# Optimization experiments

Measured on AMD Instinct MI355X. Metric: run time of the kernel, lower is better.

The kernel has to match this reference:

```python
import jax, jax.numpy as jnp
import numpy as np

H = 1024        # hidden_size
V = 50257       # output_size (vocab)
L = 2048        # number of encoder annotations


def setup_inputs() -> dict:
    key = jax.random.key(0)
    ks = jax.random.split(key, 24)
    s = 0.02
    inp = {
        "input_tok": jax.random.randint(ks[0], (1,), 0, V),
        "hidden": jax.random.normal(ks[1], (1, H), jnp.float32),
        "encoder_outputs": jax.random.normal(ks[2], (L, 1, 2 * H), jnp.float32),
        "cell_state": jax.random.normal(ks[3], (1, H), jnp.float32),
        # embedding: Linear(V, H)
        "W_emb": jax.random.normal(ks[4], (V, H), jnp.float32) * s,
        "b_emb": jnp.zeros((H,), jnp.float32),
        # attn_layer: Linear(3H, H); attn_output: Linear(H, 1)
        "W_attn": jax.random.normal(ks[5], (3 * H, H), jnp.float32) * s,
        "b_attn": jnp.zeros((H,), jnp.float32),
        "W_attn_out": jax.random.normal(ks[6], (H, 1), jnp.float32) * s,
        "b_attn_out": jnp.zeros((1,), jnp.float32),
        # LSTM gates: Linear(3H + H, H) each
        "W_i": jax.random.normal(ks[7], (4 * H, H), jnp.float32) * s,
        "b_i": jnp.zeros((H,), jnp.float32),
        "W_o": jax.random.normal(ks[8], (4 * H, H), jnp.float32) * s,
        "b_o": jnp.zeros((H,), jnp.float32),
        "W_f": jax.random.normal(ks[9], (4 * H, H), jnp.float32) * s,
        "b_f": jnp.zeros((H,), jnp.float32),
        "W_c": jax.random.normal(ks[10], (4 * H, H), jnp.float32) * s,
        "b_c": jnp.zeros((H,), jnp.float32),
        # output_layer: Linear(4H, V)
        "W_out": jax.random.normal(ks[11], (4 * H, V), jnp.float32) * s,
        "b_out": jnp.zeros((V,), jnp.float32),
    }
    return inp


def reference(input_tok, hidden, encoder_outputs, cell_state,
              W_emb, b_emb, W_attn, b_attn, W_attn_out, b_attn_out,
              W_i, b_i, W_o, b_o, W_f, b_f, W_c, b_c, W_out, b_out):
    # embedding of one-hot previous token: [1, V] @ [V, H] -> [1, H]
    one_hot = jax.nn.one_hot(input_tok, V, dtype=W_emb.dtype)
    emb = one_hot @ W_emb + b_emb                     # [1, H]
    # dropout_p = 0.0 -> identity (eval-mode reference)

    enc = encoder_outputs[:, 0, :]                    # [L, 2H]
    hid_b = jnp.broadcast_to(hidden, (enc.shape[0], hidden.shape[1]))
    attn_in = jnp.concatenate([enc, hid_b], axis=1)   # [L, 3H]
    scores = jnp.tanh(attn_in @ W_attn + b_attn) @ W_attn_out + b_attn_out  # [L, 1]
    # exp(e_ij) / sum_j exp(e_ij)  ==  softmax over encoder steps
    attn_weights = jax.nn.softmax(scores, axis=0)     # [L, 1]
    context = jnp.sum(attn_weights * enc, axis=0, keepdims=True)  # [1, 2H]

    # LSTM step on cat(embedding, context) with state (hidden, cell_state)
    lstm_in = jnp.concatenate([emb, context], axis=1)              # [1, 3H]
    combined = jnp.concatenate([lstm_in, hidden], axis=1)          # [1, 4H]
    i_g = jax.nn.sigmoid(combined @ W_i + b_i)
    o_g = jax.nn.sigmoid(combined @ W_o + b_o)
    f_g = jax.nn.sigmoid(combined @ W_f + b_f)
    c_g = jnp.tanh(combined @ W_c + b_c)
    new_cell = f_g * cell_state + i_g * c_g
    next_hidden = o_g * jnp.tanh(new_cell)

    out = jnp.concatenate([emb, hidden, context], axis=1) @ W_out + b_out  # [1, V]
    log_softmax = jax.nn.log_softmax(out, axis=1)
    return (log_softmax, next_hidden, attn_weights, new_cell)
```

## Files before the change

kernel.cpp:

```cpp
#include <hip/hip_runtime.h>
#include <hip/hip_bf16.h>
#include <math.h>

#define Hh 1024
#define Vv 50257
#define Ll 2048
#define H2 2048
#define H4 4096

#define WS_EMB  0
#define WS_SC   1024
#define WS_CTX  3072
#define WS_GATE 5120
#define WS_LOG  9216
#define WS_PAIR 59474
#define WS_LOGZ 59868
#define WS_HB   59872
#define OA_BYTES 245760u
#define OB_BYTES 8634368u

#define OUT_NH Vv
#define OUT_AW (Vv + 1024)
#define OUT_NC (Vv + 3072)

typedef __attribute__((ext_vector_type(8))) short bf16x8;
typedef __attribute__((ext_vector_type(4))) float f32x4;
typedef __attribute__((ext_vector_type(4), aligned(4))) float f32x4u;

__device__ __forceinline__ float sigmoidf_(float x) { return 1.f / (1.f + expf(-x)); }
__device__ __forceinline__ unsigned short f2bf(float f) {
    union { float f; unsigned u; } v; v.f = f;
    unsigned r = v.u + 0x7FFF + ((v.u >> 16) & 1);
    return (unsigned short)(r >> 16);
}

__global__ void k1_prep(const int* __restrict__ tok, const float* __restrict__ W_emb,
                        const float* __restrict__ b_emb, const float* __restrict__ b_out,
                        const float* __restrict__ b_attn, float* __restrict__ ws) {
    int i = blockIdx.x * 256 + threadIdx.x;
    if (i < Hh)  ws[WS_EMB + i] = W_emb[(size_t)tok[0] * Hh + i] + b_emb[i];
    if (i < Hh)  ws[WS_HB + i] = b_attn[i];
    if (i < Ll)  ws[WS_SC + i] = 0.f;
    if (i < H2)  ws[WS_CTX + i] = 0.f;
    if (i < H4)  ws[WS_GATE + i] = 0.f;
    if (i < Vv)  ws[WS_LOG + i] = b_out[i];
}

__global__ __launch_bounds__(256) void kPrep(const float* __restrict__ enc,
        const float* __restrict__ W_attn, const float* __restrict__ hidden,
        float* __restrict__ ws, char* __restrict__ wsb) {
    __shared__ union { float a[16][132]; float b[32][68]; } sh;
    int bx = blockIdx.x;
    int t = threadIdx.x;
    if (bx < 2048) {
        int mt = bx >> 4, kc = bx & 15;
        {
            int row = t >> 4, c8 = (t & 15) * 8;
            const float* src = enc + (size_t)(mt * 16 + row) * H2 + kc * 128 + c8;
            float4 v0 = *(const float4*)src;
            float4 v1 = *(const float4*)(src + 4);
            *(float4*)&sh.a[row][c8] = v0;
            *(float4*)&sh.a[row][c8 + 4] = v1;
        }
        __syncthreads();
        int ktl = t >> 6, l = t & 63;
        int r2 = l & 15, k8 = (l >> 4) * 8;
        bf16x8 o;
#pragma unroll
        for (int j = 0; j < 8; ++j) o[j] = (short)f2bf(sh.a[r2][ktl * 32 + k8 + j]);
        *(bf16x8*)(wsb + OA_BYTES + ((size_t)(mt * 64 + kc * 4 + ktl)) * 1024 + l * 16) = o;
    } else if (bx < 3072) {
        int bxx = bx - 2048;
        int kt = bxx >> 4, nc = bxx & 15;
        {
            int r = t >> 3, c8 = (t & 7) * 8;
            const float* src = W_attn + (size_t)(kt * 32 + r) * Hh + nc * 64 + c8;
            float4 v0 = *(const float4*)src;
            float4 v1 = *(const float4*)(src + 4);
            *(float4*)&sh.b[r][c8] = v0;
            *(float4*)&sh.b[r][c8 + 4] = v1;
        }
        __syncthreads();
        int ntl = t >> 6, l = t & 63;
        int col = ntl * 16 + (l & 15), k8 = (l >> 4) * 8;
        bf16x8 o;
#pragma unroll
        for (int j = 0; j < 8; ++j) o[j] = (short)f2bf(sh.b[k8 + j][col]);
        *(bf16x8*)(wsb + OB_BYTES + ((size_t)((nc * 4 + ntl) * 64 + kt)) * 1024 + l * 16) = o;
    } else {
        int bxx = bx - 3072;
        int hc = bxx & 3, kc = bxx >> 2;
        int h = hc * 256 + t;
        int k0 = kc * 16;
        const float* p = W_attn + (size_t)(H2 + k0) * Hh + h;
        float acc = 0.f;
#pragma unroll
        for (int k = 0; k < 16; ++k) { acc += hidden[k0 + k] * __builtin_nontemporal_load(p); p += Hh; }
        atomicAdd(&ws[WS_HB + h], acc);
    }
}

__global__ __launch_bounds__(128, 1) void kG(const char* __restrict__ wsb,
        const float* __restrict__ Wo, float* __restrict__ ws) {
    int bx = blockIdx.x;
    int bm = bx >> 4, bn = bx & 15;
    int t = threadIdx.x, w = t >> 6, l = t & 63;
    int mt0 = bm * 4 + w * 2;
    int nt0 = bn * 4;
    const char* pa0 = wsb + OA_BYTES + (size_t)(mt0)     * 65536 + l * 16;
    const char* pa1 = wsb + OA_BYTES + (size_t)(mt0 + 1) * 65536 + l * 16;
    const char* pb0 = wsb + OB_BYTES + (size_t)(nt0)     * 65536 + l * 16;
    const char* pb1 = wsb + OB_BYTES + (size_t)(nt0 + 1) * 65536 + l * 16;
    const char* pb2 = wsb + OB_BYTES + (size_t)(nt0 + 2) * 65536 + l * 16;
    const char* pb3 = wsb + OB_BYTES + (size_t)(nt0 + 3) * 65536 + l * 16;

    f32x4 acc[2][4];
#pragma unroll
    for (int i = 0; i < 2; ++i)
#pragma unroll
        for (int j = 0; j < 4; ++j) acc[i][j] = (f32x4){0.f, 0.f, 0.f, 0.f};

    bf16x8 As[8][2], Bs[8][4];
#define LOADK(s, kk) { int o_ = (kk) * 1024; \
    As[s][0] = *(const bf16x8*)(pa0 + o_); As[s][1] = *(const bf16x8*)(pa1 + o_); \
    Bs[s][0] = *(const bf16x8*)(pb0 + o_); Bs[s][1] = *(const bf16x8*)(pb1 + o_); \
    Bs[s][2] = *(const bf16x8*)(pb2 + o_); Bs[s][3] = *(const bf16x8*)(pb3 + o_); }
#define MFMAK(s) { \
    _Pragma("unroll") for (int mr = 0; mr < 2; ++mr) \
    _Pragma("unroll") for (int nr = 0; nr < 4; ++nr) \
        acc[mr][nr] = __builtin_amdgcn_mfma_f32_16x16x32_bf16(As[s][mr], Bs[s][nr], acc[mr][nr], 0, 0, 0); }

    LOADK(0, 0) LOADK(1, 1) LOADK(2, 2) LOADK(3, 3)
    LOADK(4, 4) LOADK(5, 5) LOADK(6, 6) LOADK(7, 7)
    for (int kt = 0; kt < 56; kt += 8) {
        MFMAK(0) LOADK(0, kt + 8)
        MFMAK(1) LOADK(1, kt + 9)
        MFMAK(2) LOADK(2, kt + 10)
        MFMAK(3) LOADK(3, kt + 11)
        MFMAK(4) LOADK(4, kt + 12)
        MFMAK(5) LOADK(5, kt + 13)
        MFMAK(6) LOADK(6, kt + 14)
        MFMAK(7) LOADK(7, kt + 15)
    }
    MFMAK(0) MFMAK(1) MFMAK(2) MFMAK(3) MFMAK(4) MFMAK(5) MFMAK(6) MFMAK(7)
#undef LOADK
#undef MFMAK

    float sp[8];
#pragma unroll
    for (int i = 0; i < 8; ++i) sp[i] = 0.f;
    int nlane = bn * 64 + (l & 15);
#pragma unroll
    for (int nr = 0; nr < 4; ++nr) {
        int n = nlane + nr * 16;
        float hb = ws[WS_HB + n];
        float wo = Wo[n];
#pragma unroll
        for (int mr = 0; mr < 2; ++mr)
#pragma unroll
            for (int r = 0; r < 4; ++r)
                sp[mr * 4 + r] += tanhf(acc[mr][nr][r] + hb) * wo;
    }
#pragma unroll
    for (int m = 1; m <= 8; m <<= 1)
#pragma unroll
        for (int i = 0; i < 8; ++i) sp[i] += __shfl_xor(sp[i], m, 64);
    if ((l & 15) == 0) {
        int mbase = bm * 64 + w * 32 + (l >> 4) * 4;
#pragma unroll
        for (int mr = 0; mr < 2; ++mr)
#pragma unroll
            for (int r = 0; r < 4; ++r)
                atomicAdd(&ws[WS_SC + mbase + mr * 16 + r], sp[mr * 4 + r]);
    }
}

__global__ __launch_bounds__(256) void k34(const float* __restrict__ enc,
        float* __restrict__ ws, float* __restrict__ out) {
    __shared__ float red[256];
    __shared__ float wl[64];
    int b = blockIdx.x, t = threadIdx.x;
    int jc = b & 7, lc = b >> 3;
    float s[8];
    float mx = -INFINITY;
#pragma unroll
    for (int i = 0; i < 8; ++i) { s[i] = ws[WS_SC + i * 256 + t]; mx = fmaxf(mx, s[i]); }
    red[t] = mx;
    __syncthreads();
    for (int off = 128; off > 0; off >>= 1) {
        if (t < off) red[t] = fmaxf(red[t], red[t + off]);
        __syncthreads();
    }
    float M = red[0];
    __syncthreads();
    float se = 0.f;
#pragma unroll
    for (int i = 0; i < 8; ++i) se += expf(s[i] - M);
    red[t] = se;
    __syncthreads();
    for (int off = 128; off > 0; off >>= 1) {
        if (t < off) red[t] += red[t + off];
        __syncthreads();
    }
    float invZ = 1.f / red[0];
    int l0 = lc * 64;
    if (t < 64) wl[t] = expf(ws[WS_SC + l0 + t] - M) * invZ;
    __syncthreads();
    if (jc == 0 && t < 64) out[OUT_AW + l0 + t] = wl[t];
    int j = jc * 256 + t;
    float acc = 0.f;
#pragma unroll 8
    for (int i = 0; i < 64; ++i)
        acc += wl[i] * enc[(size_t)(l0 + i) * H2 + j];
    atomicAdd(&ws[WS_CTX + j], acc);
}

__global__ __launch_bounds__(256) void k5k7(const float* __restrict__ W_out,
        const float* __restrict__ W_i, const float* __restrict__ W_o,
        const float* __restrict__ W_f, const float* __restrict__ W_c,
        const float* __restrict__ hidden, float* __restrict__ ws) {
    int bx = blockIdx.x, t = threadIdx.x;
    if (bx < 800) {
        __shared__ float xs[256];
        int vb = bx % 50, kc = bx / 50;
        int k0 = kc * 256;
        {
            int k = k0 + t;
            xs[t] = (k < 1024) ? ws[WS_EMB + k] : (k < 2048) ? hidden[k - 1024] : ws[WS_CTX + (k - 2048)];
        }
        __syncthreads();
        int v4 = vb * 1024 + t * 4;
        if (v4 + 3 < Vv) {
            const char* p = (const char*)(W_out + (size_t)k0 * Vv + v4);
            f32x4 a = (f32x4){0.f, 0.f, 0.f, 0.f};
#pragma unroll 4
            for (int i = 0; i < 256; ++i) {
                f32x4u wv = __builtin_nontemporal_load((const f32x4u*)p);
                a += wv * xs[i];
                p += (size_t)Vv * 4;
            }
            atomicAdd(&ws[WS_LOG + v4 + 0], a.x);
            atomicAdd(&ws[WS_LOG + v4 + 1], a.y);
            atomicAdd(&ws[WS_LOG + v4 + 2], a.z);
            atomicAdd(&ws[WS_LOG + v4 + 3], a.w);
        } else if (v4 < Vv) {
            for (int jj = 0; jj < 4 && v4 + jj < Vv; ++jj) {
                const float* p = W_out + (size_t)k0 * Vv + v4 + jj;
                float a = 0.f;
                for (int i = 0; i < 256; ++i) { a += xs[i] * (*p); p += Vv; }
                atomicAdd(&ws[WS_LOG + v4 + jj], a);
            }
        }
    } else {
        int bxx = bx - 800;
        int g = bxx & 3, kc = bxx >> 2;
        int k0 = kc * 32;
        const float* Wm = (g == 0) ? W_i : (g == 1) ? W_o : (g == 2) ? W_f : W_c;
        const f32x4* p = (const f32x4*)(Wm + (size_t)k0 * Hh) + t;
        f32x4 a = (f32x4){0.f, 0.f, 0.f, 0.f};
#pragma unroll 8
        for (int k = k0; k < k0 + 32; ++k) {
            float x = (k < 1024) ? ws[WS_EMB + k] : (k < 3072) ? ws[WS_CTX + (k - 1024)] : hidden[k - 3072];
            f32x4 wv = __builtin_nontemporal_load(p);
            a += wv * x;
            p += 256;
        }
        int h4 = t * 4;
        atomicAdd(&ws[WS_GATE + g * 1024 + h4 + 0], a.x);
        atomicAdd(&ws[WS_GATE + g * 1024 + h4 + 1], a.y);
        atomicAdd(&ws[WS_GATE + g * 1024 + h4 + 2], a.z);
        atomicAdd(&ws[WS_GATE + g * 1024 + h4 + 3], a.w);
    }
}

__global__ __launch_bounds__(256) void k6k8a(const float* __restrict__ b_i,
        const float* __restrict__ b_o, const float* __restrict__ b_f,
        const float* __restrict__ b_c, const float* __restrict__ cell,
        float* __restrict__ ws, float* __restrict__ out) {
    int bx = blockIdx.x, t = threadIdx.x;
    if (bx < 197) {
        __shared__ float sm[256];
        int v = bx * 256 + t;
        float x = (v < Vv) ? ws[WS_LOG + v] : -INFINITY;
        sm[t] = x;
        __syncthreads();
        for (int off = 128; off > 0; off >>= 1) {
            if (t < off) sm[t] = fmaxf(sm[t], sm[t + off]);
            __syncthreads();
        }
        float m = sm[0];
        __syncthreads();
        sm[t] = (v < Vv) ? expf(x - m) : 0.f;
        __syncthreads();
        for (int off = 128; off > 0; off >>= 1) {
            if (t < off) sm[t] += sm[t + off];
            __syncthreads();
        }
        if (t == 0) { ws[WS_PAIR + 2 * bx] = m; ws[WS_PAIR + 2 * bx + 1] = sm[0]; }
    } else {
#pragma unroll
        for (int r = 0; r < 4; ++r) {
            int h = t + r * 256;
            float ig = sigmoidf_(ws[WS_GATE + h] + b_i[h]);
            float og = sigmoidf_(ws[WS_GATE + 1024 + h] + b_o[h]);
            float fg = sigmoidf_(ws[WS_GATE + 2048 + h] + b_f[h]);
            float cg = tanhf(ws[WS_GATE + 3072 + h] + b_c[h]);
            float nc = fg * cell[h] + ig * cg;
            out[OUT_NC + h] = nc;
            out[OUT_NH + h] = og * tanhf(nc);
        }
    }
}

__global__ __launch_bounds__(256) void k8bc(const float* __restrict__ ws, float* __restrict__ out) {
    __shared__ float sm[256], ss[256];
    int t = threadIdx.x;
    float m = (t < 197) ? ws[WS_PAIR + 2 * t] : -INFINITY;
    float s = (t < 197) ? ws[WS_PAIR + 2 * t + 1] : 0.f;
    sm[t] = m;
    __syncthreads();
    for (int off = 128; off > 0; off >>= 1) {
        if (t < off) sm[t] = fmaxf(sm[t], sm[t + off]);
        __syncthreads();
    }
    float M = sm[0];
    ss[t] = s * expf(m - M);
    __syncthreads();
    for (int off = 128; off > 0; off >>= 1) {
        if (t < off) ss[t] += ss[t + off];
        __syncthreads();
    }
    float logZ = M + logf(ss[0]);
    int v = blockIdx.x * 256 + t;
    if (v < Vv) out[v] = ws[WS_LOG + v] - logZ;
}

extern "C" void kernel_launch(void* const* d_in, const int* in_sizes, int n_in,
                              void* d_out, int out_size, void* d_ws, size_t ws_size,
                              hipStream_t stream) {
    const int*   tok        = (const int*)d_in[0];
    const float* hidden     = (const float*)d_in[1];
    const float* enc        = (const float*)d_in[2];
    const float* cell       = (const float*)d_in[3];
    const float* W_emb      = (const float*)d_in[4];
    const float* b_emb      = (const float*)d_in[5];
    const float* W_attn     = (const float*)d_in[6];
    const float* b_attn     = (const float*)d_in[7];
    const float* W_attn_out = (const float*)d_in[8];
    const float* W_i   = (const float*)d_in[10];
    const float* b_i   = (const float*)d_in[11];
    const float* W_o   = (const float*)d_in[12];
    const float* b_o   = (const float*)d_in[13];
    const float* W_f   = (const float*)d_in[14];
    const float* b_f   = (const float*)d_in[15];
    const float* W_c   = (const float*)d_in[16];
    const float* b_c   = (const float*)d_in[17];
    const float* W_out = (const float*)d_in[18];
    const float* b_out = (const float*)d_in[19];
    float* out = (float*)d_out;
    float* ws  = (float*)d_ws;
    char*  wsb = (char*)d_ws;

    k1_prep<<<dim3(197), dim3(256), 0, stream>>>(tok, W_emb, b_emb, b_out, b_attn, ws);
    kPrep<<<dim3(3328), dim3(256), 0, stream>>>(enc, W_attn, hidden, ws, wsb);
    kG<<<dim3(512), dim3(128), 0, stream>>>(wsb, W_attn_out, ws);
    k34<<<dim3(256), dim3(256), 0, stream>>>(enc, ws, out);
    k5k7<<<dim3(1312), dim3(256), 0, stream>>>(W_out, W_i, W_o, W_f, W_c, hidden, ws);
    k6k8a<<<dim3(198), dim3(256), 0, stream>>>(b_i, b_o, b_f, b_c, cell, ws, out);
    k8bc<<<dim3(197), dim3(256), 0, stream>>>(ws, out);
}
```

Baseline: 224.7 us.

## Spread W_out streaming across earlier kernels and replace logit atomics with partials

The large W_out GEMV, previously one phase after the attention pipeline, is split by K-chunk. Each chunk is issued inside whichever earlier kernel already has its input available: hidden and embedding chunks go in the prep kernels, embedding chunks also share the MFMA scoring kernel and the softmax/context kernel, and context chunks go in the gate kernel. This overlaps the bandwidth-bound weight stream with the attention GEMM and softmax stages. The atomic accumulation into the logits is replaced by per-chunk partial rows in workspace, which the log-softmax kernel sums together with b_out. The cost is extra workspace traffic for 16 partial rows and heterogeneous blocks that may unbalance the compute-bound kernels.

Result: slower. 291.5 us (+29.7%).

```diff
diff --git a/kernel.cpp b/kernel.cpp
--- a/kernel.cpp
+++ b/kernel.cpp
@@ -14,10 +14,11 @@
 #define WS_GATE 5120
 #define WS_LOG  9216
 #define WS_PAIR 59474
-#define WS_LOGZ 59868
 #define WS_HB   59872
 #define OA_BYTES 245760u
 #define OB_BYTES 8634368u
+#define PP 50264
+#define WS_PART_F 3210240
 
 #define OUT_NH Vv
 #define OUT_AW (Vv + 1024)
@@ -34,24 +35,56 @@
     return (unsigned short)(r >> 16);
 }
 
-__global__ void k1_prep(const int* __restrict__ tok, const float* __restrict__ W_emb,
-                        const float* __restrict__ b_emb, const float* __restrict__ b_out,
-                        const float* __restrict__ b_attn, float* __restrict__ ws) {
-    int i = blockIdx.x * 256 + threadIdx.x;
-    if (i < Hh)  ws[WS_EMB + i] = W_emb[(size_t)tok[0] * Hh + i] + b_emb[i];
-    if (i < Hh)  ws[WS_HB + i] = b_attn[i];
-    if (i < Ll)  ws[WS_SC + i] = 0.f;
-    if (i < H2)  ws[WS_CTX + i] = 0.f;
-    if (i < H4)  ws[WS_GATE + i] = 0.f;
-    if (i < Vv)  ws[WS_LOG + i] = b_out[i];
-}
-
-__global__ __launch_bounds__(256) void kPrep(const float* __restrict__ enc,
+__device__ __forceinline__ void stream_wout(const float* __restrict__ W_out,
+        const float* __restrict__ xs, int k0, int v4, float* __restrict__ part_row) {
+    if (v4 + 3 < Vv) {
+        const char* p = (const char*)(W_out + (size_t)k0 * Vv + v4);
+        f32x4 a = (f32x4){0.f, 0.f, 0.f, 0.f};
+#pragma unroll 4
+        for (int i = 0; i < 256; ++i) {
+            f32x4u wv = __builtin_nontemporal_load((const f32x4u*)p);
+            a += wv * xs[i];
+            p += (size_t)Vv * 4;
+        }
+        __builtin_nontemporal_store(a, (f32x4u*)(part_row + v4));
+    } else if (v4 < Vv) {
+        for (int jj = 0; jj < 4 && v4 + jj < Vv; ++jj) {
+            const float* p = W_out + (size_t)k0 * Vv + v4 + jj;
+            float a = 0.f;
+            for (int i = 0; i < 256; ++i) { a += xs[i] * (*p); p += Vv; }
+            part_row[v4 + jj] = a;
+        }
+    }
+}
+
+__global__ __launch_bounds__(256) void kA(const int* __restrict__ tok,
+        const float* __restrict__ W_emb, const float* __restrict__ b_emb,
+        const float* __restrict__ b_attn, const float* __restrict__ hidden,
+        const float* __restrict__ W_out, float* __restrict__ ws) {
+    __shared__ float xs[256];
+    int bx = blockIdx.x, t = threadIdx.x;
+    if (bx < 16) {
+        int i = bx * 256 + t;
+        if (i < Hh) { ws[WS_EMB + i] = W_emb[(size_t)tok[0] * Hh + i] + b_emb[i];
+                      ws[WS_HB + i] = b_attn[i]; }
+        if (i < Ll)  ws[WS_SC + i] = 0.f;
+        if (i < H2)  ws[WS_CTX + i] = 0.f;
+        if (i < H4)  ws[WS_GATE + i] = 0.f;
+    } else {
+        int s = bx - 16;
+        int kc = 4 + s / 50, vb = s % 50;
+        int k0 = kc * 256;
+        xs[t] = hidden[k0 - 1024 + t];
+        __syncthreads();
+        stream_wout(W_out, xs, k0, vb * 1024 + t * 4, ws + WS_PART_F + (size_t)kc * PP);
+    }
+}
+
+__global__ __launch_bounds__(256) void kB(const float* __restrict__ enc,
         const float* __restrict__ W_attn, const float* __restrict__ hidden,
-        float* __restrict__ ws, char* __restrict__ wsb) {
-    __shared__ union { float a[16][132]; float b[32][68]; } sh;
-    int bx = blockIdx.x;
-    int t = threadIdx.x;
+        const float* __restrict__ W_out, float* __restrict__ ws, char* __restrict__ wsb) {
+    __shared__ union { float a[16][132]; float b[32][68]; float xs[256]; } sh;
+    int bx = blockIdx.x, t = threadIdx.x;
     if (bx < 2048) {
         int mt = bx >> 4, kc = bx & 15;
         {
@@ -87,7 +120,7 @@
 #pragma unroll
         for (int j = 0; j < 8; ++j) o[j] = (short)f2bf(sh.b[k8 + j][col]);
         *(bf16x8*)(wsb + OB_BYTES + ((size_t)((nc * 4 + ntl) * 64 + kt)) * 1024 + l * 16) = o;
-    } else {
+    } else if (bx < 3328) {
         int bxx = bx - 3072;
         int hc = bxx & 3, kc = bxx >> 2;
         int h = hc * 256 + t;
@@ -97,30 +130,41 @@
 #pragma unroll
         for (int k = 0; k < 16; ++k) { acc += hidden[k0 + k] * __builtin_nontemporal_load(p); p += Hh; }
         atomicAdd(&ws[WS_HB + h], acc);
-    }
-}
-
-__global__ __launch_bounds__(128, 1) void kG(const char* __restrict__ wsb,
-        const float* __restrict__ Wo, float* __restrict__ ws) {
-    int bx = blockIdx.x;
-    int bm = bx >> 4, bn = bx & 15;
-    int t = threadIdx.x, w = t >> 6, l = t & 63;
-    int mt0 = bm * 4 + w * 2;
-    int nt0 = bn * 4;
-    const char* pa0 = wsb + OA_BYTES + (size_t)(mt0)     * 65536 + l * 16;
-    const char* pa1 = wsb + OA_BYTES + (size_t)(mt0 + 1) * 65536 + l * 16;
-    const char* pb0 = wsb + OB_BYTES + (size_t)(nt0)     * 65536 + l * 16;
-    const char* pb1 = wsb + OB_BYTES + (size_t)(nt0 + 1) * 65536 + l * 16;
-    const char* pb2 = wsb + OB_BYTES + (size_t)(nt0 + 2) * 65536 + l * 16;
-    const char* pb3 = wsb + OB_BYTES + (size_t)(nt0 + 3) * 65536 + l * 16;
-
-    f32x4 acc[2][4];
-#pragma unroll
-    for (int i = 0; i < 2; ++i)
-#pragma unroll
-        for (int j = 0; j < 4; ++j) acc[i][j] = (f32x4){0.f, 0.f, 0.f, 0.f};
-
-    bf16x8 As[8][2], Bs[8][4];
+    } else {
+        int s = bx - 3328;
+        int kc = (s < 50) ? 7 : 0;
+        int vb = s % 50;
+        int k0 = kc * 256;
+        sh.xs[t] = (kc == 7) ? hidden[768 + t] : ws[WS_EMB + t];
+        __syncthreads();
+        stream_wout(W_out, sh.xs, k0, vb * 1024 + t * 4, ws + WS_PART_F + (size_t)kc * PP);
+    }
+}
+
+__global__ __launch_bounds__(128, 1) void kC(const char* __restrict__ wsb,
+        const float* __restrict__ Wo, const float* __restrict__ W_out,
+        float* __restrict__ ws) {
+    __shared__ float xs[256];
+    int bx = blockIdx.x, t = threadIdx.x;
+    if (bx < 512) {
+        int bm = bx >> 4, bn = bx & 15;
+        int w = t >> 6, l = t & 63;
+        int mt0 = bm * 4 + w * 2;
+        int nt0 = bn * 4;
+        const char* pa0 = wsb + OA_BYTES + (size_t)(mt0)     * 65536 + l * 16;
+        const char* pa1 = wsb + OA_BYTES + (size_t)(mt0 + 1) * 65536 + l * 16;
+        const char* pb0 = wsb + OB_BYTES + (size_t)(nt0)     * 65536 + l * 16;
+        const char* pb1 = wsb + OB_BYTES + (size_t)(nt0 + 1) * 65536 + l * 16;
+        const char* pb2 = wsb + OB_BYTES + (size_t)(nt0 + 2) * 65536 + l * 16;
+        const char* pb3 = wsb + OB_BYTES + (size_t)(nt0 + 3) * 65536 + l * 16;
+
+        f32x4 acc[2][4];
+#pragma unroll
+        for (int i = 0; i < 2; ++i)
+#pragma unroll
+            for (int j = 0; j < 4; ++j) acc[i][j] = (f32x4){0.f, 0.f, 0.f, 0.f};
+
+        bf16x8 As[8][2], Bs[8][4];
 #define LOADK(s, kk) { int o_ = (kk) * 1024; \
     As[s][0] = *(const bf16x8*)(pa0 + o_); As[s][1] = *(const bf16x8*)(pa1 + o_); \
     Bs[s][0] = *(const bf16x8*)(pb0 + o_); Bs[s][1] = *(const bf16x8*)(pb1 + o_); \
@@ -130,129 +174,122 @@
     _Pragma("unroll") for (int nr = 0; nr < 4; ++nr) \
         acc[mr][nr] = __builtin_amdgcn_mfma_f32_16x16x32_bf16(As[s][mr], Bs[s][nr], acc[mr][nr], 0, 0, 0); }
 
-    LOADK(0, 0) LOADK(1, 1) LOADK(2, 2) LOADK(3, 3)
-    LOADK(4, 4) LOADK(5, 5) LOADK(6, 6) LOADK(7, 7)
-    for (int kt = 0; kt < 56; kt += 8) {
-        MFMAK(0) LOADK(0, kt + 8)
-        MFMAK(1) LOADK(1, kt + 9)
-        MFMAK(2) LOADK(2, kt + 10)
-        MFMAK(3) LOADK(3, kt + 11)
-        MFMAK(4) LOADK(4, kt + 12)
-        MFMAK(5) LOADK(5, kt + 13)
-        MFMAK(6) LOADK(6, kt + 14)
-        MFMAK(7) LOADK(7, kt + 15)
-    }
-    MFMAK(0) MFMAK(1) MFMAK(2) MFMAK(3) MFMAK(4) MFMAK(5) MFMAK(6) MFMAK(7)
+        LOADK(0, 0) LOADK(1, 1) LOADK(2, 2) LOADK(3, 3)
+        LOADK(4, 4) LOADK(5, 5) LOADK(6, 6) LOADK(7, 7)
+        for (int kt = 0; kt < 56; kt += 8) {
+            MFMAK(0) LOADK(0, kt + 8)
+            MFMAK(1) LOADK(1, kt + 9)
+            MFMAK(2) LOADK(2, kt + 10)
+            MFMAK(3) LOADK(3, kt + 11)
+            MFMAK(4) LOADK(4, kt + 12)
+            MFMAK(5) LOADK(5, kt + 13)
+            MFMAK(6) LOADK(6, kt + 14)
+            MFMAK(7) LOADK(7, kt + 15)
+        }
+        MFMAK(0) MFMAK(1) MFMAK(2) MFMAK(3) MFMAK(4) MFMAK(5) MFMAK(6) MFMAK(7)
 #undef LOADK
 #undef MFMAK
 
-    float sp[8];
-#pragma unroll
-    for (int i = 0; i < 8; ++i) sp[i] = 0.f;
-    int nlane = bn * 64 + (l & 15);
-#pragma unroll
-    for (int nr = 0; nr < 4; ++nr) {
-        int n = nlane + nr * 16;
-        float hb = ws[WS_HB + n];
-        float wo = Wo[n];
-#pragma unroll
-        for (int mr = 0; mr < 2; ++mr)
-#pragma unroll
-            for (int r = 0; r < 4; ++r)
-                sp[mr * 4 + r] += tanhf(acc[mr][nr][r] + hb) * wo;
-    }
-#pragma unroll
-    for (int m = 1; m <= 8; m <<= 1)
-#pragma unroll
-        for (int i = 0; i < 8; ++i) sp[i] += __shfl_xor(sp[i], m, 64);
-    if ((l & 15) == 0) {
-        int mbase = bm * 64 + w * 32 + (l >> 4) * 4;
-#pragma unroll
-        for (int mr = 0; mr < 2; ++mr)
-#pragma unroll
-            for (int r = 0; r < 4; ++r)
-                atomicAdd(&ws[WS_SC + mbase + mr * 16 + r], sp[mr * 4 + r]);
-    }
-}
-
-__global__ __launch_bounds__(256) void k34(const float* __restrict__ enc,
-        float* __restrict__ ws, float* __restrict__ out) {
+        float sp[8];
+#pragma unroll
+        for (int i = 0; i < 8; ++i) sp[i] = 0.f;
+        int nlane = bn * 64 + (l & 15);
+#pragma unroll
+        for (int nr = 0; nr < 4; ++nr) {
+            int n = nlane + nr * 16;
+            float hb = ws[WS_HB + n];
+            float wo = Wo[n];
+#pragma unroll
+            for (int mr = 0; mr < 2; ++mr)
+#pragma unroll
+                for (int r = 0; r < 4; ++r)
+                    sp[mr * 4 + r] += tanhf(acc[mr][nr][r] + hb) * wo;
+        }
+#pragma unroll
+        for (int m = 1; m <= 8; m <<= 1)
+#pragma unroll
+            for (int i = 0; i < 8; ++i) sp[i] += __shfl_xor(sp[i], m, 64);
+        if ((l & 15) == 0) {
+            int mbase = bm * 64 + w * 32 + (l >> 4) * 4;
+#pragma unroll
+            for (int mr = 0; mr < 2; ++mr)
+#pragma unroll
+                for (int r = 0; r < 4; ++r)
+                    atomicAdd(&ws[WS_SC + mbase + mr * 16 + r], sp[mr * 4 + r]);
+        }
+    } else {
+        int s = bx - 512;
+        int kc = 1 + s / 99, vb = s % 99;
+        int k0 = kc * 256;
+        xs[t] = ws[WS_EMB + k0 + t];
+        xs[t + 128] = ws[WS_EMB + k0 + t + 128];
+        __syncthreads();
+        stream_wout(W_out, xs, k0, vb * 512 + t * 4, ws + WS_PART_F + (size_t)kc * PP);
+    }
+}
+
+__global__ __launch_bounds__(256) void kD(const float* __restrict__ enc,
+        const float* __restrict__ W_out, float* __restrict__ ws, float* __restrict__ out) {
     __shared__ float red[256];
     __shared__ float wl[64];
-    int b = blockIdx.x, t = threadIdx.x;
-    int jc = b & 7, lc = b >> 3;
-    float s[8];
-    float mx = -INFINITY;
-#pragma unroll
-    for (int i = 0; i < 8; ++i) { s[i] = ws[WS_SC + i * 256 + t]; mx = fmaxf(mx, s[i]); }
-    red[t] = mx;
-    __syncthreads();
-    for (int off = 128; off > 0; off >>= 1) {
-        if (t < off) red[t] = fmaxf(red[t], red[t + off]);
-        __syncthreads();
-    }
-    float M = red[0];
-    __syncthreads();
-    float se = 0.f;
-#pragma unroll
-    for (int i = 0; i < 8; ++i) se += expf(s[i] - M);
-    red[t] = se;
-    __syncthreads();
-    for (int off = 128; off > 0; off >>= 1) {
-        if (t < off) red[t] += red[t + off];
-        __syncthreads();
-    }
-    float invZ = 1.f / red[0];
-    int l0 = lc * 64;
-    if (t < 64) wl[t] = expf(ws[WS_SC + l0 + t] - M) * invZ;
-    __syncthreads();
-    if (jc == 0 && t < 64) out[OUT_AW + l0 + t] = wl[t];
-    int j = jc * 256 + t;
-    float acc = 0.f;
+    __shared__ float xs[256];
+    int bx = blockIdx.x, t = threadIdx.x;
+    if (bx < 256) {
+        int jc = bx & 7, lc = bx >> 3;
+        float s[8];
+        float mx = -INFINITY;
+#pragma unroll
+        for (int i = 0; i < 8; ++i) { s[i] = ws[WS_SC + i * 256 + t]; mx = fmaxf(mx, s[i]); }
+        red[t] = mx;
+        __syncthreads();
+        for (int off = 128; off > 0; off >>= 1) {
+            if (t < off) red[t] = fmaxf(red[t], red[t + off]);
+            __syncthreads();
+        }
+        float M = red[0];
+        __syncthreads();
+        float se = 0.f;
+#pragma unroll
+        for (int i = 0; i < 8; ++i) se += expf(s[i] - M);
+        red[t] = se;
+        __syncthreads();
+        for (int off = 128; off > 0; off >>= 1) {
+            if (t < off) red[t] += red[t + off];
+            __syncthreads();
+        }
+        float invZ = 1.f / red[0];
+        int l0 = lc * 64;
+        if (t < 64) wl[t] = expf(ws[WS_SC + l0 + t] - M) * invZ;
+        __syncthreads();
+        if (jc == 0 && t < 64) out[OUT_AW + l0 + t] = wl[t];
+        int j = jc * 256 + t;
+        float acc = 0.f;
 #pragma unroll 8
-    for (int i = 0; i < 64; ++i)
-        acc += wl[i] * enc[(size_t)(l0 + i) * H2 + j];
-    atomicAdd(&ws[WS_CTX + j], acc);
-}
-
-__global__ __launch_bounds__(256) void k5k7(const float* __restrict__ W_out,
+        for (int i = 0; i < 64; ++i)
+            acc += wl[i] * enc[(size_t)(l0 + i) * H2 + j];
+        atomicAdd(&ws[WS_CTX + j], acc);
+    } else {
+        int vb = bx - 256;
+        xs[t] = ws[WS_EMB + 768 + t];
+        __syncthreads();
+        stream_wout(W_out, xs, 768, vb * 1024 + t * 4, ws + WS_PART_F + (size_t)3 * PP);
+    }
+}
+
+__global__ __launch_bounds__(256) void kE(const float* __restrict__ W_out,
         const float* __restrict__ W_i, const float* __restrict__ W_o,
         const float* __restrict__ W_f, const float* __restrict__ W_c,
         const float* __restrict__ hidden, float* __restrict__ ws) {
-    int bx = blockIdx.x, t = threadIdx.x;
-    if (bx < 800) {
-        __shared__ float xs[256];
-        int vb = bx % 50, kc = bx / 50;
+    __shared__ float xs[256];
+    int bx = blockIdx.x, t = threadIdx.x;
+    if (bx < 400) {
+        int kc = 8 + bx / 50, vb = bx % 50;
         int k0 = kc * 256;
-        {
-            int k = k0 + t;
-            xs[t] = (k < 1024) ? ws[WS_EMB + k] : (k < 2048) ? hidden[k - 1024] : ws[WS_CTX + (k - 2048)];
-        }
-        __syncthreads();
-        int v4 = vb * 1024 + t * 4;
-        if (v4 + 3 < Vv) {
-            const char* p = (const char*)(W_out + (size_t)k0 * Vv + v4);
-            f32x4 a = (f32x4){0.f, 0.f, 0.f, 0.f};
-#pragma unroll 4
-            for (int i = 0; i < 256; ++i) {
-                f32x4u wv = __builtin_nontemporal_load((const f32x4u*)p);
-                a += wv * xs[i];
-                p += (size_t)Vv * 4;
-            }
-            atomicAdd(&ws[WS_LOG + v4 + 0], a.x);
-            atomicAdd(&ws[WS_LOG + v4 + 1], a.y);
-            atomicAdd(&ws[WS_LOG + v4 + 2], a.z);
-            atomicAdd(&ws[WS_LOG + v4 + 3], a.w);
-        } else if (v4 < Vv) {
-            for (int jj = 0; jj < 4 && v4 + jj < Vv; ++jj) {
-                const float* p = W_out + (size_t)k0 * Vv + v4 + jj;
-                float a = 0.f;
-                for (int i = 0; i < 256; ++i) { a += xs[i] * (*p); p += Vv; }
-                atomicAdd(&ws[WS_LOG + v4 + jj], a);
-            }
-        }
-    } else {
-        int bxx = bx - 800;
+        xs[t] = ws[WS_CTX + k0 - 2048 + t];
+        __syncthreads();
+        stream_wout(W_out, xs, k0, vb * 1024 + t * 4, ws + WS_PART_F + (size_t)kc * PP);
+    } else {
+        int bxx = bx - 400;
         int g = bxx & 3, kc = bxx >> 2;
         int k0 = kc * 32;
         const float* Wm = (g == 0) ? W_i : (g == 1) ? W_o : (g == 2) ? W_f : W_c;
@@ -273,15 +310,22 @@
     }
 }
 
-__global__ __launch_bounds__(256) void k6k8a(const float* __restrict__ b_i,
+__global__ __launch_bounds__(256) void kF(const float* __restrict__ b_i,
         const float* __restrict__ b_o, const float* __restrict__ b_f,
         const float* __restrict__ b_c, const float* __restrict__ cell,
-        float* __restrict__ ws, float* __restrict__ out) {
+        const float* __restrict__ b_out, float* __restrict__ ws, float* __restrict__ out) {
     int bx = blockIdx.x, t = threadIdx.x;
     if (bx < 197) {
         __shared__ float sm[256];
         int v = bx * 256 + t;
-        float x = (v < Vv) ? ws[WS_LOG + v] : -INFINITY;
+        float x = -INFINITY;
+        if (v < Vv) {
+            x = b_out[v];
+            const float* pp = ws + WS_PART_F + v;
+#pragma unroll
+            for (int kc = 0; kc < 16; ++kc) x += pp[(size_t)kc * PP];
+            ws[WS_LOG + v] = x;
+        }
         sm[t] = x;
         __syncthreads();
         for (int off = 128; off > 0; off >>= 1) {
@@ -361,11 +405,11 @@
     float* ws  = (float*)d_ws;
     char*  wsb = (char*)d_ws;
 
-    k1_prep<<<dim3(197), dim3(256), 0, stream>>>(tok, W_emb, b_emb, b_out, b_attn, ws);
-    kPrep<<<dim3(3328), dim3(256), 0, stream>>>(enc, W_attn, hidden, ws, wsb);
-    kG<<<dim3(512), dim3(128), 0, stream>>>(wsb, W_attn_out, ws);
-    k34<<<dim3(256), dim3(256), 0, stream>>>(enc, ws, out);
-    k5k7<<<dim3(1312), dim3(256), 0, stream>>>(W_out, W_i, W_o, W_f, W_c, hidden, ws);
-    k6k8a<<<dim3(198), dim3(256), 0, stream>>>(b_i, b_o, b_f, b_c, cell, ws, out);
+    kA<<<dim3(166), dim3(256), 0, stream>>>(tok, W_emb, b_emb, b_attn, hidden, W_out, ws);
+    kB<<<dim3(3428), dim3(256), 0, stream>>>(enc, W_attn, hidden, W_out, ws, wsb);
+    kC<<<dim3(710), dim3(128), 0, stream>>>(wsb, W_attn_out, W_out, ws);
+    kD<<<dim3(306), dim3(256), 0, stream>>>(enc, W_out, ws, out);
+    kE<<<dim3(912), dim3(256), 0, stream>>>(W_out, W_i, W_o, W_f, W_c, hidden, ws);
+    kF<<<dim3(198), dim3(256), 0, stream>>>(b_i, b_o, b_f, b_c, cell, b_out, ws, out);
     k8bc<<<dim3(197), dim3(256), 0, stream>>>(ws, out);
 }
```
